# Kernel optimization log

Hardware: AMD Instinct MI355X
Metric: run time of the kernel (lower is better)

The kernel has to match this reference:

```python
import jax, jax.numpy as jnp
import numpy as np

EPS = 1e-6


def _ring_view(t, start, length, M):
    # contiguous logical view of `length` oldest positions starting at start
    if start + length <= M:
        return t[:, start:start + length]
    first = t[:, start:]
    return jnp.concatenate([first, t[:, :length - first.shape[1]]], axis=1)


def _ring_write(t, start, chunk, M):
    # write chunk at logical position `start`, wrapping around the ring
    C = chunk.shape[1]
    if start + C <= M:
        return t.at[:, start:start + C].set(chunk)
    first = M - start
    t = t.at[:, start:].set(chunk[:, :first])
    return t.at[:, :C - first].set(chunk[:, first:])


def setup_inputs() -> dict:
    key = jax.random.key(0)
    ks = jax.random.split(key, 9)
    B, M, Hh, D, F, C = 4, 1088, 32, 128, 128, 512
    f = lambda k, s: jax.random.normal(k, s, dtype=jnp.float32)
    return {
        "K": f(ks[0], (B, M, Hh, D)),
        "V": f(ks[1], (B, M, Hh, D)),
        "FK": f(ks[2], (B, M, Hh, F)),
        "H": f(ks[3], (B, Hh, F, D)),
        "S": f(ks[4], (B, Hh, F)),
        "k_c": f(ks[5], (B, C, Hh, D)),
        "v_c": f(ks[6], (B, C, Hh, D)),
        "fk_c": f(ks[7], (B, C, Hh, F)),
        "fq": f(ks[8], (B, C, Hh, F)),
        "write_ptr": 100,
        "valid": 1088,
    }


def reference(K, V, FK, H, S, k_c, v_c, fk_c, fq, write_ptr, valid):
    M = K.shape[1]
    C = k_c.shape[1]
    if valid + C <= M:
        # room left in ring buffer: plain write, no eviction
        pos = (write_ptr + valid) % M
        K = _ring_write(K, pos, k_c, M)
        V = _ring_write(V, pos, v_c, M)
        FK = _ring_write(FK, pos, fk_c, M)
    else:
        # evict num_excess oldest tokens into recurrent state H, S
        num_excess = valid + C - M
        old_fk = _ring_view(FK, write_ptr, num_excess, M)  # (B, E, H, F)
        old_v = _ring_view(V, write_ptr, num_excess, M)    # (B, E, H, D)
        H = H + jnp.einsum('behf,behd->bhfd', old_fk, old_v)
        S = S + old_fk.sum(axis=1)
        write_ptr = (write_ptr + num_excess) % M
        pos = (write_ptr + M) % M  # valid == M now
        K = _ring_write(K, pos, k_c, M)
        V = _ring_write(V, pos, v_c, M)
        FK = _ring_write(FK, pos, fk_c, M)
    # linear_attn_forward(fq)
    y_num = jnp.einsum('bchf,bhfd->bchd', fq, H)
    y_den = jnp.einsum('bchf,bhf->bch', fq, S)[..., None]
    return y_num, y_den, K, V, FK, H, S
```

## Files before the change

### kernel.cpp

```cpp
#include <hip/hip_runtime.h>

typedef float f32x4 __attribute__((ext_vector_type(4)));

constexpr int B  = 4;
constexpr int M  = 1088;
constexpr int HH = 32;
constexpr int D  = 128;
constexpr int F  = 128;
constexpr int C  = 512;

constexpr int SZ_YNUM = B * C * HH * D;
constexpr int SZ_YDEN = B * C * HH;
constexpr int SZ_KVM  = B * M * HH * D;
constexpr int SZ_H    = B * HH * F * D;

constexpr int OFF_YNUM = 0;
constexpr int OFF_YDEN = OFF_YNUM + SZ_YNUM;
constexpr int OFF_K    = OFF_YDEN + SZ_YDEN;
constexpr int OFF_V    = OFF_K + SZ_KVM;
constexpr int OFF_FK   = OFF_V + SZ_KVM;
constexpr int OFF_H    = OFF_FK + SZ_KVM;
constexpr int OFF_S    = OFF_H + SZ_H;

constexpr int INNER4      = HH * D / 4;
constexpr int ROWS_PER_CB = 4;
constexpr int COPY_BLOCKS = B * M / ROWS_PER_CB;
constexpr int HS_BLOCKS   = B * HH * 2;
constexpr int Y_BLOCKS    = B * HH * 8;

__device__ __forceinline__ void ring_params(const int* wp_p, const int* valid_p,
                                            int& wp, int& num_excess, int& pos) {
    wp = *wp_p;
    int valid = *valid_p;
    if (valid + C <= M) {
        num_excess = 0;
        pos = (wp + valid) % M;
    } else {
        num_excess = valid + C - M;
        pos = (wp + num_excess) % M;
    }
}

__device__ __forceinline__ void ring_copy_block(int cb, int tid,
                                                const f32x4* __restrict__ src,
                                                const f32x4* __restrict__ chk,
                                                f32x4* __restrict__ dst,
                                                int pos) {
    int bm0 = cb * ROWS_PER_CB;
#pragma unroll
    for (int r = 0; r < ROWS_PER_CB; ++r) {
        int bm = bm0 + r;
        int m = bm % M;
        int b = bm / M;
        int off = m - pos;
        if (off < 0) off += M;
        const f32x4* s = (off < C) ? &chk[(b * C + off) * INNER4]
                                   : &src[bm * INNER4];
        f32x4* d = &dst[bm * INNER4];
        f32x4 t0 = __builtin_nontemporal_load(s + tid);
        f32x4 t1 = __builtin_nontemporal_load(s + 256 + tid);
        f32x4 t2 = __builtin_nontemporal_load(s + 512 + tid);
        f32x4 t3 = __builtin_nontemporal_load(s + 768 + tid);
        __builtin_nontemporal_store(t0, d + tid);
        __builtin_nontemporal_store(t1, d + 256 + tid);
        __builtin_nontemporal_store(t2, d + 512 + tid);
        __builtin_nontemporal_store(t3, d + 768 + tid);
    }
}

constexpr int ESTEP = 32;

__device__ void update_hs_body(int bx,
                               const float* __restrict__ FKi,
                               const float* __restrict__ Vi,
                               const float* __restrict__ Hi,
                               const float* __restrict__ Si,
                               float* __restrict__ Ho,
                               float* __restrict__ So,
                               int wp, int num_excess) {
    const int tid = threadIdx.x;
    const int fhalf = bx & 1;
    const int bh = bx >> 1;
    const int h = bh & (HH - 1);
    const int b = bh >> 5;
    const int fbase = fhalf * 64;

    __shared__ float  fk_s[ESTEP][64];
    __shared__ f32x4  v_s[ESTEP][32];
    __shared__ float  sred[4][64];

    const int tf = tid >> 5;
    const int td = tid & 31;
    const int cq = tid & 63;
    const int qq = tid >> 6;

    f32x4 acc[8];
#pragma unroll
    for (int i = 0; i < 8; ++i) acc[i] = (f32x4)0.f;
    float s_part = 0.f;

    float fk_r[8];
    f32x4 v_r[4];

    auto load_tile = [&](int e0) {
#pragma unroll
        for (int j = 0; j < 8; ++j) {
            int e = e0 + qq + 4 * j;
            int me = wp + e;
            if (me >= M) me -= M;
            if (me >= M) me -= M;
            float v = 0.f;
            if (e < num_excess) v = FKi[((b * M + me) * HH + h) * F + fbase + cq];
            fk_r[j] = v;
        }
#pragma unroll
        for (int j = 0; j < 4; ++j) {
            int e = e0 + tf + 8 * j;
            int me = wp + e;
            if (me >= M) me -= M;
            if (me >= M) me -= M;
            f32x4 v = (f32x4)0.f;
            if (e < num_excess) v = *(const f32x4*)&Vi[((b * M + me) * HH + h) * D + td * 4];
            v_r[j] = v;
        }
    };
    auto store_tile = [&]() {
#pragma unroll
        for (int j = 0; j < 8; ++j) fk_s[qq + 4 * j][cq] = fk_r[j];
#pragma unroll
        for (int j = 0; j < 4; ++j) v_s[tf + 8 * j][td] = v_r[j];
    };

    if (num_excess > 0) {
        load_tile(0);
        store_tile();
        for (int e0 = 0; e0 < num_excess; e0 += ESTEP) {
            bool more = (e0 + ESTEP < num_excess);
            if (more) load_tile(e0 + ESTEP);
            __syncthreads();
#pragma unroll
            for (int ee = 0; ee < ESTEP; ++ee) {
                f32x4 fa = *(const f32x4*)&fk_s[ee][tf * 8];
                f32x4 fb = *(const f32x4*)&fk_s[ee][tf * 8 + 4];
                f32x4 vv = v_s[ee][td];
                acc[0] += fa.x * vv; acc[1] += fa.y * vv;
                acc[2] += fa.z * vv; acc[3] += fa.w * vv;
                acc[4] += fb.x * vv; acc[5] += fb.y * vv;
                acc[6] += fb.z * vv; acc[7] += fb.w * vv;
            }
#pragma unroll
            for (int j = 0; j < 8; ++j) s_part += fk_s[qq * 8 + j][cq];
            __syncthreads();
            if (more) store_tile();
        }
    }

    sred[qq][cq] = s_part;
    __syncthreads();
    if (tid < 64) {
        int f = fbase + tid;
        int si = (b * HH + h) * F + f;
        So[si] = Si[si] + sred[0][tid] + sred[1][tid] + sred[2][tid] + sred[3][tid];
    }

#pragma unroll
    for (int i = 0; i < 8; ++i) {
        int f = fbase + tf * 8 + i;
        int base = ((b * HH + h) * F + f) * D + td * 4;
        f32x4 hold = __builtin_nontemporal_load((const f32x4*)&Hi[base]);
        *(f32x4*)&Ho[base] = hold + acc[i];
    }
}

__device__ void compute_y_den_body(int bx,
                                   const float* __restrict__ fq,
                                   const float* __restrict__ Hn,
                                   const float* __restrict__ Sn,
                                   float* __restrict__ ynum,
                                   float* __restrict__ yden) {
    const int tid = threadIdx.x;
    int t = bx;
    const int ct = t & 7; t >>= 3;
    const int h = t & (HH - 1);
    const int b = t >> 5;
    const int c0 = ct * 64;

    __shared__ float  fq_s[32][65];
    __shared__ f32x4  h_s[32][32];
    __shared__ float  S_s[128];
    __shared__ float  den_s[64][4];

    const int tc = tid >> 5;
    const int td = tid & 31;
    const int cq = tid & 63;
    const int qq = tid >> 6;

    if (tid < 128) S_s[tid] = Sn[(b * HH + h) * F + tid];

    f32x4 acc[8];
#pragma unroll
    for (int i = 0; i < 8; ++i) acc[i] = (f32x4)0.f;
    float den_part = 0.f;

    for (int f0 = 0; f0 < F; f0 += 32) {
#pragma unroll
        for (int r = 0; r < 8; ++r) {
            int idx = tid + r * 256;
            int cc = idx >> 5, ee = idx & 31;
            fq_s[ee][cc] = __builtin_nontemporal_load(
                &fq[((b * C + c0 + cc) * HH + h) * F + f0 + ee]);
        }
#pragma unroll
        for (int r = 0; r < 4; ++r) {
            int idx = tid + r * 256;
            int row = idx >> 5, col = idx & 31;
            h_s[row][col] = *(const f32x4*)&Hn[((b * HH + h) * F + f0 + row) * D + col * 4];
        }
        __syncthreads();
#pragma unroll
        for (int ee = 0; ee < 32; ++ee) {
            f32x4 hv = h_s[ee][td];
#pragma unroll
            for (int i = 0; i < 8; ++i) {
                float q = fq_s[ee][tc * 8 + i];
                acc[i] += q * hv;
            }
        }
#pragma unroll
        for (int j = 0; j < 8; ++j)
            den_part += fq_s[qq * 8 + j][cq] * S_s[f0 + qq * 8 + j];
        __syncthreads();
    }

    den_s[cq][qq] = den_part;
    __syncthreads();
    if (tid < 64)
        yden[(b * C + c0 + tid) * HH + h] =
            den_s[tid][0] + den_s[tid][1] + den_s[tid][2] + den_s[tid][3];

#pragma unroll
    for (int i = 0; i < 8; ++i) {
        int c = c0 + tc * 8 + i;
        int base = ((b * C + c) * HH + h) * D + td * 4;
        __builtin_nontemporal_store(acc[i], (f32x4*)&ynum[base]);
    }
}

__global__ __launch_bounds__(256) void fused_hs_copy(
        const float* __restrict__ FKi, const float* __restrict__ Vi,
        const float* __restrict__ Hi,  const float* __restrict__ Si,
        float* __restrict__ Ho,        float* __restrict__ So,
        const f32x4* __restrict__ V4,  const f32x4* __restrict__ vc,  f32x4* __restrict__ oV,
        const f32x4* __restrict__ FK4, const f32x4* __restrict__ fkc, f32x4* __restrict__ oFK,
        const f32x4* __restrict__ K4,  const f32x4* __restrict__ kc,  f32x4* __restrict__ oK,
        const int* __restrict__ wp_p,  const int* __restrict__ valid_p) {
    int wp, num_excess, pos;
    ring_params(wp_p, valid_p, wp, num_excess, pos);

    int bx = blockIdx.x;
    if (bx < HS_BLOCKS) {
        update_hs_body(bx, FKi, Vi, Hi, Si, Ho, So, wp, num_excess);
        return;
    }
    bx -= HS_BLOCKS;
    if (bx < COPY_BLOCKS) {
        ring_copy_block(bx, threadIdx.x, V4, vc, oV, pos);
        return;
    }
    bx -= COPY_BLOCKS;
    if (bx < COPY_BLOCKS) {
        ring_copy_block(bx, threadIdx.x, FK4, fkc, oFK, pos);
        return;
    }
    bx -= COPY_BLOCKS;
    ring_copy_block(bx, threadIdx.x, K4, kc, oK, pos);
}

__global__ __launch_bounds__(256) void fused_y(
        const float* __restrict__ fq, const float* __restrict__ Hn,
        const float* __restrict__ Sn,
        float* __restrict__ ynum,     float* __restrict__ yden) {
    compute_y_den_body(blockIdx.x, fq, Hn, Sn, ynum, yden);
}

extern "C" void kernel_launch(void* const* d_in, const int* in_sizes, int n_in,
                              void* d_out, int out_size, void* d_ws, size_t ws_size,
                              hipStream_t stream) {
    const float* K   = (const float*)d_in[0];
    const float* V   = (const float*)d_in[1];
    const float* FK  = (const float*)d_in[2];
    const float* H   = (const float*)d_in[3];
    const float* S   = (const float*)d_in[4];
    const float* k_c = (const float*)d_in[5];
    const float* v_c = (const float*)d_in[6];
    const float* fk_c= (const float*)d_in[7];
    const float* fq  = (const float*)d_in[8];
    const int* wp    = (const int*)d_in[9];
    const int* valid = (const int*)d_in[10];

    float* out = (float*)d_out;
    float* o_ynum = out + OFF_YNUM;
    float* o_yden = out + OFF_YDEN;
    float* o_K    = out + OFF_K;
    float* o_V    = out + OFF_V;
    float* o_FK   = out + OFF_FK;
    float* o_H    = out + OFF_H;
    float* o_S    = out + OFF_S;

    fused_hs_copy<<<HS_BLOCKS + 3 * COPY_BLOCKS, 256, 0, stream>>>(
        FK, V, H, S, o_H, o_S,
        (const f32x4*)V,  (const f32x4*)v_c,  (f32x4*)o_V,
        (const f32x4*)FK, (const f32x4*)fk_c, (f32x4*)o_FK,
        (const f32x4*)K,  (const f32x4*)k_c,  (f32x4*)o_K,
        wp, valid);

    fused_y<<<Y_BLOCKS, 256, 0, stream>>>(fq, o_H, o_S, o_ynum, o_yden);
}
```

Measured before the change: 139.7 us.

## Move K ring copy into y kernel, double-buffer HS and y tile loads

Moves the K ring-buffer copy from the first kernel into the second so the memory-bound copy can overlap the y_num/y_den compute and balance work between the launches. Switches the H/S update loop to two shared-memory buffers with register prefetch so only one barrier is needed per tile. Adds register prefetch of the next fq/H tile in the y kernel. Replaces nontemporal loads and stores with plain ones. This uses more shared memory and registers, which may lower occupancy, and changes cache behaviour for the streaming copies.

```diff
diff --git a/kernel.cpp b/kernel.cpp
--- a/kernel.cpp
+++ b/kernel.cpp
@@ -57,14 +57,9 @@
         const f32x4* s = (off < C) ? &chk[(b * C + off) * INNER4]
                                    : &src[bm * INNER4];
         f32x4* d = &dst[bm * INNER4];
-        f32x4 t0 = __builtin_nontemporal_load(s + tid);
-        f32x4 t1 = __builtin_nontemporal_load(s + 256 + tid);
-        f32x4 t2 = __builtin_nontemporal_load(s + 512 + tid);
-        f32x4 t3 = __builtin_nontemporal_load(s + 768 + tid);
-        __builtin_nontemporal_store(t0, d + tid);
-        __builtin_nontemporal_store(t1, d + 256 + tid);
-        __builtin_nontemporal_store(t2, d + 512 + tid);
-        __builtin_nontemporal_store(t3, d + 768 + tid);
+#pragma unroll
+        for (int k = 0; k < INNER4 / 256; ++k)
+            d[k * 256 + tid] = s[k * 256 + tid];
     }
 }
 
@@ -85,8 +80,8 @@
     const int b = bh >> 5;
     const int fbase = fhalf * 64;
 
-    __shared__ float  fk_s[ESTEP][64];
-    __shared__ f32x4  v_s[ESTEP][32];
+    __shared__ float  fk_s[2][ESTEP][64];
+    __shared__ f32x4  v_s[2][ESTEP][32];
     __shared__ float  sred[4][64];
 
     const int tf = tid >> 5;
@@ -99,10 +94,10 @@
     for (int i = 0; i < 8; ++i) acc[i] = (f32x4)0.f;
     float s_part = 0.f;
 
-    float fk_r[8];
-    f32x4 v_r[4];
-
-    auto load_tile = [&](int e0) {
+    float fkA[8], fkB[8];
+    f32x4 vA[4],  vB[4];
+
+    auto load_tile = [&](int e0, float* fk_r, f32x4* v_r) {
 #pragma unroll
         for (int j = 0; j < 8; ++j) {
             int e = e0 + qq + 4 * j;
@@ -124,34 +119,42 @@
             v_r[j] = v;
         }
     };
-    auto store_tile = [&]() {
-#pragma unroll
-        for (int j = 0; j < 8; ++j) fk_s[qq + 4 * j][cq] = fk_r[j];
-#pragma unroll
-        for (int j = 0; j < 4; ++j) v_s[tf + 8 * j][td] = v_r[j];
+    auto store_tile = [&](const float* fk_r, const f32x4* v_r, int buf) {
+#pragma unroll
+        for (int j = 0; j < 8; ++j) fk_s[buf][qq + 4 * j][cq] = fk_r[j];
+#pragma unroll
+        for (int j = 0; j < 4; ++j) v_s[buf][tf + 8 * j][td] = v_r[j];
+    };
+    auto compute = [&](int buf) {
+#pragma unroll
+        for (int ee = 0; ee < ESTEP; ++ee) {
+            f32x4 fa = *(const f32x4*)&fk_s[buf][ee][tf * 8];
+            f32x4 fb = *(const f32x4*)&fk_s[buf][ee][tf * 8 + 4];
+            f32x4 vv = v_s[buf][ee][td];
+            acc[0] += fa.x * vv; acc[1] += fa.y * vv;
+            acc[2] += fa.z * vv; acc[3] += fa.w * vv;
+            acc[4] += fb.x * vv; acc[5] += fb.y * vv;
+            acc[6] += fb.z * vv; acc[7] += fb.w * vv;
+        }
+#pragma unroll
+        for (int j = 0; j < 8; ++j) s_part += fk_s[buf][qq * 8 + j][cq];
     };
 
     if (num_excess > 0) {
-        load_tile(0);
-        store_tile();
-        for (int e0 = 0; e0 < num_excess; e0 += ESTEP) {
-            bool more = (e0 + ESTEP < num_excess);
-            if (more) load_tile(e0 + ESTEP);
+        const int nt = (num_excess + ESTEP - 1) / ESTEP;
+        load_tile(0, fkA, vA);
+        if (nt > 1) load_tile(ESTEP, fkB, vB);
+        store_tile(fkA, vA, 0);
+        for (int t = 0; t < nt; t += 2) {
             __syncthreads();
-#pragma unroll
-            for (int ee = 0; ee < ESTEP; ++ee) {
-                f32x4 fa = *(const f32x4*)&fk_s[ee][tf * 8];
-                f32x4 fb = *(const f32x4*)&fk_s[ee][tf * 8 + 4];
-                f32x4 vv = v_s[ee][td];
-                acc[0] += fa.x * vv; acc[1] += fa.y * vv;
-                acc[2] += fa.z * vv; acc[3] += fa.w * vv;
-                acc[4] += fb.x * vv; acc[5] += fb.y * vv;
-                acc[6] += fb.z * vv; acc[7] += fb.w * vv;
-            }
-#pragma unroll
-            for (int j = 0; j < 8; ++j) s_part += fk_s[qq * 8 + j][cq];
+            if (t + 1 < nt) store_tile(fkB, vB, 1);
+            if (t + 2 < nt) load_tile((t + 2) * ESTEP, fkA, vA);
+            compute(0);
+            if (t + 1 >= nt) break;
             __syncthreads();
-            if (more) store_tile();
+            if (t + 2 < nt) store_tile(fkA, vA, 0);
+            if (t + 3 < nt) load_tile((t + 3) * ESTEP, fkB, vB);
+            compute(1);
         }
     }
 
@@ -167,7 +170,7 @@
     for (int i = 0; i < 8; ++i) {
         int f = fbase + tf * 8 + i;
         int base = ((b * HH + h) * F + f) * D + td * 4;
-        f32x4 hold = __builtin_nontemporal_load((const f32x4*)&Hi[base]);
+        f32x4 hold = *(const f32x4*)&Hi[base];
         *(f32x4*)&Ho[base] = hold + acc[i];
     }
 }
@@ -179,10 +182,10 @@
                                    float* __restrict__ ynum,
                                    float* __restrict__ yden) {
     const int tid = threadIdx.x;
-    int t = bx;
-    const int ct = t & 7; t >>= 3;
-    const int h = t & (HH - 1);
-    const int b = t >> 5;
+    int t0 = bx;
+    const int ct = t0 & 7; t0 >>= 3;
+    const int h = t0 & (HH - 1);
+    const int b = t0 >> 5;
     const int c0 = ct * 64;
 
     __shared__ float  fq_s[32][65];
@@ -202,20 +205,40 @@
     for (int i = 0; i < 8; ++i) acc[i] = (f32x4)0.f;
     float den_part = 0.f;
 
-    for (int f0 = 0; f0 < F; f0 += 32) {
+    float fqr[8];
+    f32x4 hr[4];
+    const int lcc = tid >> 5, lee = tid & 31;
+    const int lrow = tid >> 6, lcol = tid & 63;
+
+    auto load_step = [&](int f0) {
 #pragma unroll
         for (int r = 0; r < 8; ++r) {
-            int idx = tid + r * 256;
-            int cc = idx >> 5, ee = idx & 31;
-            fq_s[ee][cc] = __builtin_nontemporal_load(
-                &fq[((b * C + c0 + cc) * HH + h) * F + f0 + ee]);
+            int cc = lcc + r * 8;
+            fqr[r] = fq[((b * C + c0 + cc) * HH + h) * F + f0 + lee];
         }
 #pragma unroll
         for (int r = 0; r < 4; ++r) {
             int idx = tid + r * 256;
             int row = idx >> 5, col = idx & 31;
-            h_s[row][col] = *(const f32x4*)&Hn[((b * HH + h) * F + f0 + row) * D + col * 4];
-        }
+            hr[r] = *(const f32x4*)&Hn[((b * HH + h) * F + f0 + row) * D + col * 4];
+        }
+    };
+    auto store_step = [&]() {
+#pragma unroll
+        for (int r = 0; r < 8; ++r) fq_s[lee][lcc + r * 8] = fqr[r];
+#pragma unroll
+        for (int r = 0; r < 4; ++r) {
+            int idx = tid + r * 256;
+            int row = idx >> 5, col = idx & 31;
+            h_s[row][col] = hr[r];
+        }
+    };
+
+    load_step(0);
+    store_step();
+    for (int step = 0; step < 4; ++step) {
+        bool more = step + 1 < 4;
+        if (more) load_step((step + 1) * 32);
         __syncthreads();
 #pragma unroll
         for (int ee = 0; ee < 32; ++ee) {
@@ -228,8 +251,9 @@
         }
 #pragma unroll
         for (int j = 0; j < 8; ++j)
-            den_part += fq_s[qq * 8 + j][cq] * S_s[f0 + qq * 8 + j];
+            den_part += fq_s[qq * 8 + j][cq] * S_s[step * 32 + qq * 8 + j];
         __syncthreads();
+        if (more) store_step();
     }
 
     den_s[cq][qq] = den_part;
@@ -242,17 +266,16 @@
     for (int i = 0; i < 8; ++i) {
         int c = c0 + tc * 8 + i;
         int base = ((b * C + c) * HH + h) * D + td * 4;
-        __builtin_nontemporal_store(acc[i], (f32x4*)&ynum[base]);
-    }
-}
-
-__global__ __launch_bounds__(256) void fused_hs_copy(
+        *(f32x4*)&ynum[base] = acc[i];
+    }
+}
+
+__global__ __launch_bounds__(256) void fused_hs_vfk(
         const float* __restrict__ FKi, const float* __restrict__ Vi,
         const float* __restrict__ Hi,  const float* __restrict__ Si,
         float* __restrict__ Ho,        float* __restrict__ So,
         const f32x4* __restrict__ V4,  const f32x4* __restrict__ vc,  f32x4* __restrict__ oV,
         const f32x4* __restrict__ FK4, const f32x4* __restrict__ fkc, f32x4* __restrict__ oFK,
-        const f32x4* __restrict__ K4,  const f32x4* __restrict__ kc,  f32x4* __restrict__ oK,
         const int* __restrict__ wp_p,  const int* __restrict__ valid_p) {
     int wp, num_excess, pos;
     ring_params(wp_p, valid_p, wp, num_excess, pos);
@@ -268,19 +291,26 @@
         return;
     }
     bx -= COPY_BLOCKS;
-    if (bx < COPY_BLOCKS) {
-        ring_copy_block(bx, threadIdx.x, FK4, fkc, oFK, pos);
-        return;
-    }
-    bx -= COPY_BLOCKS;
-    ring_copy_block(bx, threadIdx.x, K4, kc, oK, pos);
-}
-
-__global__ __launch_bounds__(256) void fused_y(
+    ring_copy_block(bx, threadIdx.x, FK4, fkc, oFK, pos);
+}
+
+__global__ __launch_bounds__(256) void fused_y_k(
         const float* __restrict__ fq, const float* __restrict__ Hn,
         const float* __restrict__ Sn,
-        float* __restrict__ ynum,     float* __restrict__ yden) {
-    compute_y_den_body(blockIdx.x, fq, Hn, Sn, ynum, yden);
+        float* __restrict__ ynum,     float* __restrict__ yden,
+        const f32x4* __restrict__ K4, const f32x4* __restrict__ kc,
+        f32x4* __restrict__ oK,
+        const int* __restrict__ wp_p, const int* __restrict__ valid_p) {
+    int wp, num_excess, pos;
+    ring_params(wp_p, valid_p, wp, num_excess, pos);
+
+    int bx = blockIdx.x;
+    if (bx < Y_BLOCKS) {
+        compute_y_den_body(bx, fq, Hn, Sn, ynum, yden);
+        return;
+    }
+    bx -= Y_BLOCKS;
+    ring_copy_block(bx, threadIdx.x, K4, kc, oK, pos);
 }
 
 extern "C" void kernel_launch(void* const* d_in, const int* in_sizes, int n_in,
@@ -307,12 +337,14 @@
     float* o_H    = out + OFF_H;
     float* o_S    = out + OFF_S;
 
-    fused_hs_copy<<<HS_BLOCKS + 3 * COPY_BLOCKS, 256, 0, stream>>>(
+    fused_hs_vfk<<<HS_BLOCKS + 2 * COPY_BLOCKS, 256, 0, stream>>>(
         FK, V, H, S, o_H, o_S,
         (const f32x4*)V,  (const f32x4*)v_c,  (f32x4*)o_V,
         (const f32x4*)FK, (const f32x4*)fk_c, (f32x4*)o_FK,
-        (const f32x4*)K,  (const f32x4*)k_c,  (f32x4*)o_K,
         wp, valid);
 
-    fused_y<<<Y_BLOCKS, 256, 0, stream>>>(fq, o_H, o_S, o_ynum, o_yden);
-}
+    fused_y_k<<<Y_BLOCKS + COPY_BLOCKS, 256, 0, stream>>>(
+        fq, o_H, o_S, o_ynum, o_yden,
+        (const f32x4*)K, (const f32x4*)k_c, (f32x4*)o_K,
+        wp, valid);
+}
```

Result: slower. 158.8 us (+13.7%).

## Split H/S eviction reduction across token partitions and move K copy into second kernel

Applied to the files above, without the earlier changes.

The H/S update is split four ways over evicted tokens. Each partition writes partial sums to workspace, and the y kernel sums these partials with the old H/S while loading tiles, writing the final H/S once per (b,h). The K ring copy moves from the first kernel into the second launch to balance the memory-bound work across both kernels. Nontemporal hints are dropped on the copy, fq loads and ynum stores, and ESTEP is halved. The cost is extra workspace traffic: 4 partial H buffers are written and then reread by all 8 y blocks per head.

```diff
diff --git a/kernel.cpp b/kernel.cpp
--- a/kernel.cpp
+++ b/kernel.cpp
@@ -13,6 +13,7 @@
 constexpr int SZ_YDEN = B * C * HH;
 constexpr int SZ_KVM  = B * M * HH * D;
 constexpr int SZ_H    = B * HH * F * D;
+constexpr int SZ_S    = B * HH * F;
 
 constexpr int OFF_YNUM = 0;
 constexpr int OFF_YDEN = OFF_YNUM + SZ_YNUM;
@@ -25,7 +26,8 @@
 constexpr int INNER4      = HH * D / 4;
 constexpr int ROWS_PER_CB = 4;
 constexpr int COPY_BLOCKS = B * M / ROWS_PER_CB;
-constexpr int HS_BLOCKS   = B * HH * 2;
+constexpr int EPARTS      = 4;
+constexpr int HS_BLOCKS   = B * HH * 2 * EPARTS;
 constexpr int Y_BLOCKS    = B * HH * 8;
 
 __device__ __forceinline__ void ring_params(const int* wp_p, const int* valid_p,
@@ -57,33 +59,33 @@
         const f32x4* s = (off < C) ? &chk[(b * C + off) * INNER4]
                                    : &src[bm * INNER4];
         f32x4* d = &dst[bm * INNER4];
-        f32x4 t0 = __builtin_nontemporal_load(s + tid);
-        f32x4 t1 = __builtin_nontemporal_load(s + 256 + tid);
-        f32x4 t2 = __builtin_nontemporal_load(s + 512 + tid);
-        f32x4 t3 = __builtin_nontemporal_load(s + 768 + tid);
-        __builtin_nontemporal_store(t0, d + tid);
-        __builtin_nontemporal_store(t1, d + 256 + tid);
-        __builtin_nontemporal_store(t2, d + 512 + tid);
-        __builtin_nontemporal_store(t3, d + 768 + tid);
-    }
-}
-
-constexpr int ESTEP = 32;
-
-__device__ void update_hs_body(int bx,
-                               const float* __restrict__ FKi,
-                               const float* __restrict__ Vi,
-                               const float* __restrict__ Hi,
-                               const float* __restrict__ Si,
-                               float* __restrict__ Ho,
-                               float* __restrict__ So,
-                               int wp, int num_excess) {
+#pragma unroll
+        for (int k = 0; k < INNER4 / 256; ++k)
+            d[k * 256 + tid] = s[k * 256 + tid];
+    }
+}
+
+constexpr int ESTEP = 16;
+
+__device__ void hs_partial_body(int bx,
+                                const float* __restrict__ FKi,
+                                const float* __restrict__ Vi,
+                                float* __restrict__ wsH,
+                                float* __restrict__ wsS,
+                                int wp, int num_excess) {
     const int tid = threadIdx.x;
-    const int fhalf = bx & 1;
-    const int bh = bx >> 1;
+    const int epart = bx & (EPARTS - 1);
+    int rest = bx >> 2;
+    const int fhalf = rest & 1;
+    const int bh = rest >> 1;
     const int h = bh & (HH - 1);
     const int b = bh >> 5;
     const int fbase = fhalf * 64;
+
+    const int echunk = (num_excess + EPARTS * ESTEP - 1) / (EPARTS * ESTEP) * ESTEP;
+    const int e_lo = epart * echunk;
+    const int e_hi_raw = e_lo + echunk;
+    const int e_hi = (e_hi_raw < num_excess) ? e_hi_raw : num_excess;
 
     __shared__ float  fk_s[ESTEP][64];
     __shared__ f32x4  v_s[ESTEP][32];
@@ -99,43 +101,43 @@
     for (int i = 0; i < 8; ++i) acc[i] = (f32x4)0.f;
     float s_part = 0.f;
 
-    float fk_r[8];
-    f32x4 v_r[4];
+    float fk_r[4];
+    f32x4 v_r[2];
 
     auto load_tile = [&](int e0) {
 #pragma unroll
-        for (int j = 0; j < 8; ++j) {
+        for (int j = 0; j < 4; ++j) {
             int e = e0 + qq + 4 * j;
             int me = wp + e;
             if (me >= M) me -= M;
             if (me >= M) me -= M;
             float v = 0.f;
-            if (e < num_excess) v = FKi[((b * M + me) * HH + h) * F + fbase + cq];
+            if (e < e_hi) v = FKi[((b * M + me) * HH + h) * F + fbase + cq];
             fk_r[j] = v;
         }
 #pragma unroll
-        for (int j = 0; j < 4; ++j) {
+        for (int j = 0; j < 2; ++j) {
             int e = e0 + tf + 8 * j;
             int me = wp + e;
             if (me >= M) me -= M;
             if (me >= M) me -= M;
             f32x4 v = (f32x4)0.f;
-            if (e < num_excess) v = *(const f32x4*)&Vi[((b * M + me) * HH + h) * D + td * 4];
+            if (e < e_hi) v = *(const f32x4*)&Vi[((b * M + me) * HH + h) * D + td * 4];
             v_r[j] = v;
         }
     };
     auto store_tile = [&]() {
 #pragma unroll
-        for (int j = 0; j < 8; ++j) fk_s[qq + 4 * j][cq] = fk_r[j];
-#pragma unroll
-        for (int j = 0; j < 4; ++j) v_s[tf + 8 * j][td] = v_r[j];
+        for (int j = 0; j < 4; ++j) fk_s[qq + 4 * j][cq] = fk_r[j];
+#pragma unroll
+        for (int j = 0; j < 2; ++j) v_s[tf + 8 * j][td] = v_r[j];
     };
 
-    if (num_excess > 0) {
-        load_tile(0);
+    if (e_lo < e_hi) {
+        load_tile(e_lo);
         store_tile();
-        for (int e0 = 0; e0 < num_excess; e0 += ESTEP) {
-            bool more = (e0 + ESTEP < num_excess);
+        for (int e0 = e_lo; e0 < e_hi; e0 += ESTEP) {
+            bool more = (e0 + ESTEP < e_hi);
             if (more) load_tile(e0 + ESTEP);
             __syncthreads();
 #pragma unroll
@@ -149,7 +151,7 @@
                 acc[6] += fb.z * vv; acc[7] += fb.w * vv;
             }
 #pragma unroll
-            for (int j = 0; j < 8; ++j) s_part += fk_s[qq * 8 + j][cq];
+            for (int j = 0; j < 4; ++j) s_part += fk_s[qq * 4 + j][cq];
             __syncthreads();
             if (more) store_tile();
         }
@@ -158,32 +160,36 @@
     sred[qq][cq] = s_part;
     __syncthreads();
     if (tid < 64) {
-        int f = fbase + tid;
-        int si = (b * HH + h) * F + f;
-        So[si] = Si[si] + sred[0][tid] + sred[1][tid] + sred[2][tid] + sred[3][tid];
-    }
-
+        wsS[epart * SZ_S + (b * HH + h) * F + fbase + tid] =
+            sred[0][tid] + sred[1][tid] + sred[2][tid] + sred[3][tid];
+    }
+
+    float* wsHp = wsH + epart * SZ_H;
 #pragma unroll
     for (int i = 0; i < 8; ++i) {
         int f = fbase + tf * 8 + i;
         int base = ((b * HH + h) * F + f) * D + td * 4;
-        f32x4 hold = __builtin_nontemporal_load((const f32x4*)&Hi[base]);
-        *(f32x4*)&Ho[base] = hold + acc[i];
+        *(f32x4*)&wsHp[base] = acc[i];
     }
 }
 
 __device__ void compute_y_den_body(int bx,
                                    const float* __restrict__ fq,
-                                   const float* __restrict__ Hn,
-                                   const float* __restrict__ Sn,
+                                   const float* __restrict__ Hi,
+                                   const float* __restrict__ Si,
+                                   const float* __restrict__ wsH,
+                                   const float* __restrict__ wsS,
+                                   float* __restrict__ Ho,
+                                   float* __restrict__ So,
                                    float* __restrict__ ynum,
                                    float* __restrict__ yden) {
     const int tid = threadIdx.x;
-    int t = bx;
-    const int ct = t & 7; t >>= 3;
-    const int h = t & (HH - 1);
-    const int b = t >> 5;
+    int t0 = bx;
+    const int ct = t0 & 7; t0 >>= 3;
+    const int h = t0 & (HH - 1);
+    const int b = t0 >> 5;
     const int c0 = ct * 64;
+    const int bh = b * HH + h;
 
     __shared__ float  fq_s[32][65];
     __shared__ f32x4  h_s[32][32];
@@ -195,7 +201,13 @@
     const int cq = tid & 63;
     const int qq = tid >> 6;
 
-    if (tid < 128) S_s[tid] = Sn[(b * HH + h) * F + tid];
+    if (tid < 128) {
+        float s = Si[bh * F + tid]
+                + wsS[0 * SZ_S + bh * F + tid] + wsS[1 * SZ_S + bh * F + tid]
+                + wsS[2 * SZ_S + bh * F + tid] + wsS[3 * SZ_S + bh * F + tid];
+        S_s[tid] = s;
+        if (ct == 0) So[bh * F + tid] = s;
+    }
 
     f32x4 acc[8];
 #pragma unroll
@@ -207,14 +219,20 @@
         for (int r = 0; r < 8; ++r) {
             int idx = tid + r * 256;
             int cc = idx >> 5, ee = idx & 31;
-            fq_s[ee][cc] = __builtin_nontemporal_load(
-                &fq[((b * C + c0 + cc) * HH + h) * F + f0 + ee]);
+            fq_s[ee][cc] = fq[((b * C + c0 + cc) * HH + h) * F + f0 + ee];
         }
 #pragma unroll
         for (int r = 0; r < 4; ++r) {
             int idx = tid + r * 256;
             int row = idx >> 5, col = idx & 31;
-            h_s[row][col] = *(const f32x4*)&Hn[((b * HH + h) * F + f0 + row) * D + col * 4];
+            int base = ((bh) * F + f0 + row) * D + col * 4;
+            f32x4 v = *(const f32x4*)&Hi[base];
+            v += *(const f32x4*)&wsH[0 * SZ_H + base];
+            v += *(const f32x4*)&wsH[1 * SZ_H + base];
+            v += *(const f32x4*)&wsH[2 * SZ_H + base];
+            v += *(const f32x4*)&wsH[3 * SZ_H + base];
+            h_s[row][col] = v;
+            if (ct == 0) *(f32x4*)&Ho[base] = v;
         }
         __syncthreads();
 #pragma unroll
@@ -242,24 +260,22 @@
     for (int i = 0; i < 8; ++i) {
         int c = c0 + tc * 8 + i;
         int base = ((b * C + c) * HH + h) * D + td * 4;
-        __builtin_nontemporal_store(acc[i], (f32x4*)&ynum[base]);
-    }
-}
-
-__global__ __launch_bounds__(256) void fused_hs_copy(
+        *(f32x4*)&ynum[base] = acc[i];
+    }
+}
+
+__global__ __launch_bounds__(256) void fused_hs_vfk(
         const float* __restrict__ FKi, const float* __restrict__ Vi,
-        const float* __restrict__ Hi,  const float* __restrict__ Si,
-        float* __restrict__ Ho,        float* __restrict__ So,
+        float* __restrict__ wsH,       float* __restrict__ wsS,
         const f32x4* __restrict__ V4,  const f32x4* __restrict__ vc,  f32x4* __restrict__ oV,
         const f32x4* __restrict__ FK4, const f32x4* __restrict__ fkc, f32x4* __restrict__ oFK,
-        const f32x4* __restrict__ K4,  const f32x4* __restrict__ kc,  f32x4* __restrict__ oK,
         const int* __restrict__ wp_p,  const int* __restrict__ valid_p) {
     int wp, num_excess, pos;
     ring_params(wp_p, valid_p, wp, num_excess, pos);
 
     int bx = blockIdx.x;
     if (bx < HS_BLOCKS) {
-        update_hs_body(bx, FKi, Vi, Hi, Si, Ho, So, wp, num_excess);
+        hs_partial_body(bx, FKi, Vi, wsH, wsS, wp, num_excess);
         return;
     }
     bx -= HS_BLOCKS;
@@ -268,19 +284,28 @@
         return;
     }
     bx -= COPY_BLOCKS;
-    if (bx < COPY_BLOCKS) {
-        ring_copy_block(bx, threadIdx.x, FK4, fkc, oFK, pos);
+    ring_copy_block(bx, threadIdx.x, FK4, fkc, oFK, pos);
+}
+
+__global__ __launch_bounds__(256) void fused_y_k(
+        const float* __restrict__ fq, const float* __restrict__ Hi,
+        const float* __restrict__ Si,
+        const float* __restrict__ wsH, const float* __restrict__ wsS,
+        float* __restrict__ Ho,        float* __restrict__ So,
+        float* __restrict__ ynum,      float* __restrict__ yden,
+        const f32x4* __restrict__ K4,  const f32x4* __restrict__ kc,
+        f32x4* __restrict__ oK,
+        const int* __restrict__ wp_p,  const int* __restrict__ valid_p) {
+    int wp, num_excess, pos;
+    ring_params(wp_p, valid_p, wp, num_excess, pos);
+
+    int bx = blockIdx.x;
+    if (bx < Y_BLOCKS) {
+        compute_y_den_body(bx, fq, Hi, Si, wsH, wsS, Ho, So, ynum, yden);
         return;
     }
-    bx -= COPY_BLOCKS;
+    bx -= Y_BLOCKS;
     ring_copy_block(bx, threadIdx.x, K4, kc, oK, pos);
-}
-
-__global__ __launch_bounds__(256) void fused_y(
-        const float* __restrict__ fq, const float* __restrict__ Hn,
-        const float* __restrict__ Sn,
-        float* __restrict__ ynum,     float* __restrict__ yden) {
-    compute_y_den_body(blockIdx.x, fq, Hn, Sn, ynum, yden);
 }
 
 extern "C" void kernel_launch(void* const* d_in, const int* in_sizes, int n_in,
@@ -307,12 +332,17 @@
     float* o_H    = out + OFF_H;
     float* o_S    = out + OFF_S;
 
-    fused_hs_copy<<<HS_BLOCKS + 3 * COPY_BLOCKS, 256, 0, stream>>>(
-        FK, V, H, S, o_H, o_S,
+    float* wsH = (float*)d_ws;
+    float* wsS = wsH + EPARTS * SZ_H;
+
+    fused_hs_vfk<<<HS_BLOCKS + 2 * COPY_BLOCKS, 256, 0, stream>>>(
+        FK, V, wsH, wsS,
         (const f32x4*)V,  (const f32x4*)v_c,  (f32x4*)o_V,
         (const f32x4*)FK, (const f32x4*)fk_c, (f32x4*)o_FK,
-        (const f32x4*)K,  (const f32x4*)k_c,  (f32x4*)o_K,
         wp, valid);
 
-    fused_y<<<Y_BLOCKS, 256, 0, stream>>>(fq, o_H, o_S, o_ynum, o_yden);
-}
+    fused_y_k<<<Y_BLOCKS + COPY_BLOCKS, 256, 0, stream>>>(
+        fq, H, S, wsH, wsS, o_H, o_S, o_ynum, o_yden,
+        (const f32x4*)K, (const f32x4*)k_c, (f32x4*)o_K,
+        wp, valid);
+}
```

Result: slower. 157.5 us (+12.7%).

## Move K ring copy into second kernel and split H/S and Y work finer

Applied to the files above, without the earlier changes.

Moves the K ring-buffer copy from the first kernel into the second, so its memory traffic overlaps the y_num/y_den compute. This balances bandwidth-bound and compute-bound work across both launches. H/S blocks now cover 32 feature rows instead of 64 with a shorter eviction step, and Y blocks cover 32 chunk rows instead of 64, doubling block counts for better occupancy. Launch bounds request 8 blocks per CU, and nontemporal loads and stores are replaced with plain accesses, which may change cache behaviour on the streaming copies.

```diff
diff --git a/kernel.cpp b/kernel.cpp
--- a/kernel.cpp
+++ b/kernel.cpp
@@ -13,6 +13,7 @@
 constexpr int SZ_YDEN = B * C * HH;
 constexpr int SZ_KVM  = B * M * HH * D;
 constexpr int SZ_H    = B * HH * F * D;
+constexpr int SZ_S    = B * HH * F;
 
 constexpr int OFF_YNUM = 0;
 constexpr int OFF_YDEN = OFF_YNUM + SZ_YNUM;
@@ -25,8 +26,9 @@
 constexpr int INNER4      = HH * D / 4;
 constexpr int ROWS_PER_CB = 4;
 constexpr int COPY_BLOCKS = B * M / ROWS_PER_CB;
-constexpr int HS_BLOCKS   = B * HH * 2;
-constexpr int Y_BLOCKS    = B * HH * 8;
+constexpr int HS_BLOCKS   = B * HH * 4;
+constexpr int Y_BLOCKS    = B * HH * 16;
+constexpr int ESTEP       = 16;
 
 __device__ __forceinline__ void ring_params(const int* wp_p, const int* valid_p,
                                             int& wp, int& num_excess, int& pos) {
@@ -57,78 +59,67 @@
         const f32x4* s = (off < C) ? &chk[(b * C + off) * INNER4]
                                    : &src[bm * INNER4];
         f32x4* d = &dst[bm * INNER4];
-        f32x4 t0 = __builtin_nontemporal_load(s + tid);
-        f32x4 t1 = __builtin_nontemporal_load(s + 256 + tid);
-        f32x4 t2 = __builtin_nontemporal_load(s + 512 + tid);
-        f32x4 t3 = __builtin_nontemporal_load(s + 768 + tid);
-        __builtin_nontemporal_store(t0, d + tid);
-        __builtin_nontemporal_store(t1, d + 256 + tid);
-        __builtin_nontemporal_store(t2, d + 512 + tid);
-        __builtin_nontemporal_store(t3, d + 768 + tid);
-    }
-}
-
-constexpr int ESTEP = 32;
-
-__device__ void update_hs_body(int bx,
-                               const float* __restrict__ FKi,
-                               const float* __restrict__ Vi,
-                               const float* __restrict__ Hi,
-                               const float* __restrict__ Si,
-                               float* __restrict__ Ho,
-                               float* __restrict__ So,
-                               int wp, int num_excess) {
+#pragma unroll
+        for (int k = 0; k < INNER4 / 256; ++k)
+            d[k * 256 + tid] = s[k * 256 + tid];
+    }
+}
+
+__device__ void hs_body(int bx,
+                        const float* __restrict__ FKi,
+                        const float* __restrict__ Vi,
+                        const float* __restrict__ Hi,
+                        const float* __restrict__ Si,
+                        float* __restrict__ Ho,
+                        float* __restrict__ So,
+                        int wp, int num_excess) {
     const int tid = threadIdx.x;
-    const int fhalf = bx & 1;
-    const int bh = bx >> 1;
+    const int fq4 = bx & 3;
+    const int bh = bx >> 2;
     const int h = bh & (HH - 1);
     const int b = bh >> 5;
-    const int fbase = fhalf * 64;
-
-    __shared__ float  fk_s[ESTEP][64];
-    __shared__ f32x4  v_s[ESTEP][32];
-    __shared__ float  sred[4][64];
+    const int fbase = fq4 * 32;
+
+    __shared__ float fk_s[ESTEP][32];
+    __shared__ f32x4 v_s[ESTEP][32];
+    __shared__ float sred[8][32];
 
     const int tf = tid >> 5;
     const int td = tid & 31;
-    const int cq = tid & 63;
-    const int qq = tid >> 6;
-
-    f32x4 acc[8];
-#pragma unroll
-    for (int i = 0; i < 8; ++i) acc[i] = (f32x4)0.f;
+
+    f32x4 acc[4];
+#pragma unroll
+    for (int i = 0; i < 4; ++i) acc[i] = (f32x4)0.f;
     float s_part = 0.f;
 
-    float fk_r[8];
-    f32x4 v_r[4];
+    float fk_r[2];
+    f32x4 v_r[2];
 
     auto load_tile = [&](int e0) {
 #pragma unroll
-        for (int j = 0; j < 8; ++j) {
-            int e = e0 + qq + 4 * j;
+        for (int r = 0; r < 2; ++r) {
+            int row = tf + r * 8;
+            int e = e0 + row;
             int me = wp + e;
             if (me >= M) me -= M;
             if (me >= M) me -= M;
-            float v = 0.f;
-            if (e < num_excess) v = FKi[((b * M + me) * HH + h) * F + fbase + cq];
-            fk_r[j] = v;
-        }
-#pragma unroll
-        for (int j = 0; j < 4; ++j) {
-            int e = e0 + tf + 8 * j;
-            int me = wp + e;
-            if (me >= M) me -= M;
-            if (me >= M) me -= M;
-            f32x4 v = (f32x4)0.f;
-            if (e < num_excess) v = *(const f32x4*)&Vi[((b * M + me) * HH + h) * D + td * 4];
-            v_r[j] = v;
+            float fv = 0.f;
+            f32x4 vv = (f32x4)0.f;
+            if (e < num_excess) {
+                int rowbase = (b * M + me) * HH + h;
+                fv = FKi[rowbase * F + fbase + td];
+                vv = *(const f32x4*)&Vi[rowbase * D + td * 4];
+            }
+            fk_r[r] = fv;
+            v_r[r] = vv;
         }
     };
     auto store_tile = [&]() {
 #pragma unroll
-        for (int j = 0; j < 8; ++j) fk_s[qq + 4 * j][cq] = fk_r[j];
-#pragma unroll
-        for (int j = 0; j < 4; ++j) v_s[tf + 8 * j][td] = v_r[j];
+        for (int r = 0; r < 2; ++r) {
+            fk_s[tf + r * 8][td] = fk_r[r];
+            v_s[tf + r * 8][td] = v_r[r];
+        }
     };
 
     if (num_excess > 0) {
@@ -140,126 +131,127 @@
             __syncthreads();
 #pragma unroll
             for (int ee = 0; ee < ESTEP; ++ee) {
-                f32x4 fa = *(const f32x4*)&fk_s[ee][tf * 8];
-                f32x4 fb = *(const f32x4*)&fk_s[ee][tf * 8 + 4];
+                f32x4 fa = *(const f32x4*)&fk_s[ee][tf * 4];
                 f32x4 vv = v_s[ee][td];
-                acc[0] += fa.x * vv; acc[1] += fa.y * vv;
-                acc[2] += fa.z * vv; acc[3] += fa.w * vv;
-                acc[4] += fb.x * vv; acc[5] += fb.y * vv;
-                acc[6] += fb.z * vv; acc[7] += fb.w * vv;
+                acc[0] += fa.x * vv;
+                acc[1] += fa.y * vv;
+                acc[2] += fa.z * vv;
+                acc[3] += fa.w * vv;
             }
-#pragma unroll
-            for (int j = 0; j < 8; ++j) s_part += fk_s[qq * 8 + j][cq];
+            s_part += fk_s[tf * 2][td] + fk_s[tf * 2 + 1][td];
             __syncthreads();
             if (more) store_tile();
         }
     }
 
-    sred[qq][cq] = s_part;
+    sred[tf][td] = s_part;
     __syncthreads();
-    if (tid < 64) {
-        int f = fbase + tid;
-        int si = (b * HH + h) * F + f;
-        So[si] = Si[si] + sred[0][tid] + sred[1][tid] + sred[2][tid] + sred[3][tid];
-    }
-
-#pragma unroll
-    for (int i = 0; i < 8; ++i) {
-        int f = fbase + tf * 8 + i;
-        int base = ((b * HH + h) * F + f) * D + td * 4;
-        f32x4 hold = __builtin_nontemporal_load((const f32x4*)&Hi[base]);
+    if (tid < 32) {
+        int si = bh * F + fbase + tid;
+        float s = Si[si];
+#pragma unroll
+        for (int g = 0; g < 8; ++g) s += sred[g][tid];
+        So[si] = s;
+    }
+
+#pragma unroll
+    for (int i = 0; i < 4; ++i) {
+        int f = fbase + tf * 4 + i;
+        int base = (bh * F + f) * D + td * 4;
+        f32x4 hold = *(const f32x4*)&Hi[base];
         *(f32x4*)&Ho[base] = hold + acc[i];
     }
 }
 
-__device__ void compute_y_den_body(int bx,
-                                   const float* __restrict__ fq,
-                                   const float* __restrict__ Hn,
-                                   const float* __restrict__ Sn,
-                                   float* __restrict__ ynum,
-                                   float* __restrict__ yden) {
+__device__ void y_body(int bx,
+                       const float* __restrict__ fq,
+                       const float* __restrict__ Hn,
+                       const float* __restrict__ Sn,
+                       float* __restrict__ ynum,
+                       float* __restrict__ yden) {
     const int tid = threadIdx.x;
-    int t = bx;
-    const int ct = t & 7; t >>= 3;
-    const int h = t & (HH - 1);
-    const int b = t >> 5;
-    const int c0 = ct * 64;
-
-    __shared__ float  fq_s[32][65];
-    __shared__ f32x4  h_s[32][32];
-    __shared__ float  S_s[128];
-    __shared__ float  den_s[64][4];
+    const int ct = bx & 15;
+    const int bh = bx >> 4;
+    const int h = bh & (HH - 1);
+    const int b = bh >> 5;
+    const int c0 = ct * 32;
+
+    __shared__ float fq_s[32][33];
+    __shared__ f32x4 h_s[32][32];
+    __shared__ float S_s[128];
+    __shared__ float den_s[32][8];
 
     const int tc = tid >> 5;
     const int td = tid & 31;
-    const int cq = tid & 63;
-    const int qq = tid >> 6;
-
-    if (tid < 128) S_s[tid] = Sn[(b * HH + h) * F + tid];
-
-    f32x4 acc[8];
-#pragma unroll
-    for (int i = 0; i < 8; ++i) acc[i] = (f32x4)0.f;
+    const int cq = tid & 31;
+    const int qq = tid >> 5;
+
+    if (tid < 128) S_s[tid] = Sn[bh * F + tid];
+
+    f32x4 acc[4];
+#pragma unroll
+    for (int i = 0; i < 4; ++i) acc[i] = (f32x4)0.f;
     float den_part = 0.f;
 
     for (int f0 = 0; f0 < F; f0 += 32) {
 #pragma unroll
-        for (int r = 0; r < 8; ++r) {
+        for (int r = 0; r < 4; ++r) {
             int idx = tid + r * 256;
             int cc = idx >> 5, ee = idx & 31;
-            fq_s[ee][cc] = __builtin_nontemporal_load(
-                &fq[((b * C + c0 + cc) * HH + h) * F + f0 + ee]);
+            fq_s[ee][cc] = fq[((b * C + c0 + cc) * HH + h) * F + f0 + ee];
         }
 #pragma unroll
         for (int r = 0; r < 4; ++r) {
             int idx = tid + r * 256;
             int row = idx >> 5, col = idx & 31;
-            h_s[row][col] = *(const f32x4*)&Hn[((b * HH + h) * F + f0 + row) * D + col * 4];
+            h_s[row][col] = *(const f32x4*)&Hn[(bh * F + f0 + row) * D + col * 4];
         }
         __syncthreads();
 #pragma unroll
         for (int ee = 0; ee < 32; ++ee) {
             f32x4 hv = h_s[ee][td];
 #pragma unroll
-            for (int i = 0; i < 8; ++i) {
-                float q = fq_s[ee][tc * 8 + i];
+            for (int i = 0; i < 4; ++i) {
+                float q = fq_s[ee][tc * 4 + i];
                 acc[i] += q * hv;
             }
         }
 #pragma unroll
-        for (int j = 0; j < 8; ++j)
-            den_part += fq_s[qq * 8 + j][cq] * S_s[f0 + qq * 8 + j];
+        for (int j = 0; j < 4; ++j)
+            den_part += fq_s[qq * 4 + j][cq] * S_s[f0 + qq * 4 + j];
         __syncthreads();
     }
 
     den_s[cq][qq] = den_part;
     __syncthreads();
-    if (tid < 64)
-        yden[(b * C + c0 + tid) * HH + h] =
-            den_s[tid][0] + den_s[tid][1] + den_s[tid][2] + den_s[tid][3];
-
-#pragma unroll
-    for (int i = 0; i < 8; ++i) {
-        int c = c0 + tc * 8 + i;
+    if (tid < 32) {
+        float d = 0.f;
+#pragma unroll
+        for (int g = 0; g < 8; ++g) d += den_s[tid][g];
+        yden[(b * C + c0 + tid) * HH + h] = d;
+    }
+
+#pragma unroll
+    for (int i = 0; i < 4; ++i) {
+        int c = c0 + tc * 4 + i;
         int base = ((b * C + c) * HH + h) * D + td * 4;
-        __builtin_nontemporal_store(acc[i], (f32x4*)&ynum[base]);
-    }
-}
-
-__global__ __launch_bounds__(256) void fused_hs_copy(
+        *(f32x4*)&ynum[base] = acc[i];
+    }
+}
+
+__global__ __launch_bounds__(256, 8) void fused_hs_vfk(
         const float* __restrict__ FKi, const float* __restrict__ Vi,
         const float* __restrict__ Hi,  const float* __restrict__ Si,
         float* __restrict__ Ho,        float* __restrict__ So,
         const f32x4* __restrict__ V4,  const f32x4* __restrict__ vc,  f32x4* __restrict__ oV,
         const f32x4* __restrict__ FK4, const f32x4* __restrict__ fkc, f32x4* __restrict__ oFK,
-        const f32x4* __restrict__ K4,  const f32x4* __restrict__ kc,  f32x4* __restrict__ oK,
         const int* __restrict__ wp_p,  const int* __restrict__ valid_p) {
     int wp, num_excess, pos;
     ring_params(wp_p, valid_p, wp, num_excess, pos);
 
     int bx = blockIdx.x;
     if (bx < HS_BLOCKS) {
-        update_hs_body(bx, FKi, Vi, Hi, Si, Ho, So, wp, num_excess);
+        hs_body(bx, FKi, Vi, Hi, Si, Ho, So, wp, num_excess);
         return;
     }
     bx -= HS_BLOCKS;
@@ -268,19 +260,26 @@
         return;
     }
     bx -= COPY_BLOCKS;
-    if (bx < COPY_BLOCKS) {
-        ring_copy_block(bx, threadIdx.x, FK4, fkc, oFK, pos);
-        return;
-    }
-    bx -= COPY_BLOCKS;
-    ring_copy_block(bx, threadIdx.x, K4, kc, oK, pos);
-}
-
-__global__ __launch_bounds__(256) void fused_y(
+    ring_copy_block(bx, threadIdx.x, FK4, fkc, oFK, pos);
+}
+
+__global__ __launch_bounds__(256, 8) void fused_k_y(
         const float* __restrict__ fq, const float* __restrict__ Hn,
         const float* __restrict__ Sn,
-        float* __restrict__ ynum,     float* __restrict__ yden) {
-    compute_y_den_body(blockIdx.x, fq, Hn, Sn, ynum, yden);
+        float* __restrict__ ynum,     float* __restrict__ yden,
+        const f32x4* __restrict__ K4, const f32x4* __restrict__ kc,
+        f32x4* __restrict__ oK,
+        const int* __restrict__ wp_p, const int* __restrict__ valid_p) {
+    int wp, num_excess, pos;
+    ring_params(wp_p, valid_p, wp, num_excess, pos);
+
+    int bx = blockIdx.x;
+    if (bx < COPY_BLOCKS) {
+        ring_copy_block(bx, threadIdx.x, K4, kc, oK, pos);
+        return;
+    }
+    bx -= COPY_BLOCKS;
+    y_body(bx, fq, Hn, Sn, ynum, yden);
 }
 
 extern "C" void kernel_launch(void* const* d_in, const int* in_sizes, int n_in,
@@ -307,12 +306,14 @@
     float* o_H    = out + OFF_H;
     float* o_S    = out + OFF_S;
 
-    fused_hs_copy<<<HS_BLOCKS + 3 * COPY_BLOCKS, 256, 0, stream>>>(
+    fused_hs_vfk<<<HS_BLOCKS + 2 * COPY_BLOCKS, 256, 0, stream>>>(
         FK, V, H, S, o_H, o_S,
         (const f32x4*)V,  (const f32x4*)v_c,  (f32x4*)o_V,
         (const f32x4*)FK, (const f32x4*)fk_c, (f32x4*)o_FK,
-        (const f32x4*)K,  (const f32x4*)k_c,  (f32x4*)o_K,
         wp, valid);
 
-    fused_y<<<Y_BLOCKS, 256, 0, stream>>>(fq, o_H, o_S, o_ynum, o_yden);
-}
+    fused_k_y<<<COPY_BLOCKS + Y_BLOCKS, 256, 0, stream>>>(
+        fq, o_H, o_S, o_ynum, o_yden,
+        (const f32x4*)K, (const f32x4*)k_c, (f32x4*)o_K,
+        wp, valid);
+}
```

Measured after the change: 143.1 us. 1.02x slower.
